# Kernel optimization log

Measured on AMD Instinct MI355X. Metric: run time of the kernel, lower is better.

Reference implementation:

```python
import jax, jax.numpy as jnp
import numpy as np

# Precompute flat gather indices replicating matA's banded structure.
# Row (layer l, offset i) of matA sums d[i : i+l], for l in 1..255, i in 0..255-l.
# Equivalently diff = cumsum_pad[i+l] - cumsum_pad[i].
def _build_indices():
    lo, hi, lid = [], [], []
    for l in range(1, 256):
        n = 256 - l
        i = np.arange(n)
        lo.append(i)
        hi.append(i + l)
        lid.append(np.full(n, l - 1))
    return (np.concatenate(lo), np.concatenate(hi), np.concatenate(lid))

_IDX_LO, _IDX_HI, _LAYER_ID = _build_indices()  # each length 32640
IDX_LO = jnp.asarray(_IDX_LO)
IDX_HI = jnp.asarray(_IDX_HI)
LAYER_ID = jnp.asarray(_LAYER_ID)
# elements averaged per layer: B * (256 - l)
_COUNTS = (256 - np.arange(1, 256)).astype(np.float32)
COUNTS = jnp.asarray(_COUNTS)


def setup_inputs() -> dict:
    key = jax.random.key(0)
    k1, k2, k3 = jax.random.split(key, 3)
    B = 512
    d1layer = jax.random.normal(k1, (B, 1, 255), dtype=jnp.float32)
    hvec = jax.random.normal(k2, (B, 32640), dtype=jnp.float32)
    mask = jax.random.uniform(k3, (B, 255), dtype=jnp.float32)
    return {"d1layer": d1layer, "hvec": hvec, "mask": mask}


def reference(d1layer, hvec, mask):
    B = d1layer.shape[0]
    m = jnp.power(mask, 2.5)  # [B, 255]
    d = d1layer[:, 0, :]  # [B, 255]
    # padded cumulative sum: c[:, k] = sum_{j<k} d[:, j], shape [B, 256]
    c = jnp.concatenate(
        [jnp.zeros((B, 1), dtype=d.dtype), jnp.cumsum(d, axis=1)], axis=1
    )
    # banded windowed sums for all 32640 (layer, offset) pairs at once
    matAd = c[:, IDX_HI] - c[:, IDX_LO]  # [B, 32640]
    w = m[:, LAYER_ID]  # [B, 32640], mask[:, layer-1] broadcast over offsets
    sq = jnp.square(matAd - hvec) * w  # [B, 32640]
    per_layer_sum = jax.ops.segment_sum(
        jnp.sum(sq, axis=0), LAYER_ID, num_segments=255
    )  # [255]
    loss_layers = per_layer_sum / (COUNTS * jnp.float32(B))  # per-layer mean
    return jnp.mean(loss_layers)
```

## Files before the change

### kernel.cpp

```cpp
#include <hip/hip_runtime.h>

#define NLAYER 255
#define SEQ    256
#define TOTJ   32640
#define CHUNKS 8
#define CHUNK_J (TOTJ / CHUNKS)
#define CHUNK_F4 (CHUNK_J / 4)
#define THREADS 256

__global__ void build_table(unsigned short* __restrict__ table) {
    int l = blockIdx.x + 1;
    int n = 256 - l;
    int i = threadIdx.x;
    if (i < n) {
        int base = 256 * (l - 1) - ((l - 1) * l) / 2;
        table[base + i] = (unsigned short)((l - 1) | (i << 8));
    }
}

__global__ __launch_bounds__(THREADS) void main_kernel(
        const float* __restrict__ d1layer,
        const float* __restrict__ hvec,
        const float* __restrict__ mask,
        const unsigned short* __restrict__ table,
        float* __restrict__ partials)
{
    __shared__ float c[SEQ];
    __shared__ float w[NLAYER];
    __shared__ float red[THREADS / 64];

    const int b     = blockIdx.y;
    const int chunk = blockIdx.x;
    const int t     = threadIdx.x;

    c[t] = (t > 0) ? d1layer[b * NLAYER + (t - 1)] : 0.0f;
    if (t < NLAYER) {
        float mk = mask[b * NLAYER + t];
        w[t] = mk * mk * sqrtf(mk) / (float)(NLAYER - t);
    }
    __syncthreads();

    #pragma unroll
    for (int off = 1; off < SEQ; off <<= 1) {
        float v   = c[t];
        float add = (t >= off) ? c[t - off] : 0.0f;
        __syncthreads();
        c[t] = v + add;
        __syncthreads();
    }

    const float4* hv4 =
        (const float4*)(hvec + (size_t)b * TOTJ + (size_t)chunk * CHUNK_J);
    const unsigned short* tb = table + chunk * CHUNK_J;

    float acc = 0.0f;
    for (int f4 = t; f4 < CHUNK_F4; f4 += THREADS) {
        float4 h = hv4[f4];
        ushort4 tv = *(const ushort4*)(tb + f4 * 4);

        int l0 = tv.x & 0xFF, lo0 = tv.x >> 8;
        int l1 = tv.y & 0xFF, lo1 = tv.y >> 8;
        int l2 = tv.z & 0xFF, lo2 = tv.z >> 8;
        int l3 = tv.w & 0xFF, lo3 = tv.w >> 8;

        float d0 = (c[lo0 + l0 + 1] - c[lo0]) - h.x;
        float d1 = (c[lo1 + l1 + 1] - c[lo1]) - h.y;
        float d2 = (c[lo2 + l2 + 1] - c[lo2]) - h.z;
        float d3 = (c[lo3 + l3 + 1] - c[lo3]) - h.w;

        acc += d0 * d0 * w[l0];
        acc += d1 * d1 * w[l1];
        acc += d2 * d2 * w[l2];
        acc += d3 * d3 * w[l3];
    }

    #pragma unroll
    for (int off = 32; off > 0; off >>= 1)
        acc += __shfl_down(acc, off, 64);
    int lane = t & 63, wid = t >> 6;
    if (lane == 0) red[wid] = acc;
    __syncthreads();
    if (t == 0) {
        float s = 0.0f;
        #pragma unroll
        for (int i = 0; i < THREADS / 64; ++i) s += red[i];
        partials[b * gridDim.x + chunk] = s;
    }
}

__global__ void reduce_kernel(const float* __restrict__ partials, int n, int B,
                              float* __restrict__ out) {
    __shared__ float red[16];
    float acc = 0.0f;
    for (int i = threadIdx.x; i < n; i += blockDim.x) acc += partials[i];
    #pragma unroll
    for (int off = 32; off > 0; off >>= 1)
        acc += __shfl_down(acc, off, 64);
    int lane = threadIdx.x & 63, wid = threadIdx.x >> 6;
    if (lane == 0) red[wid] = acc;
    __syncthreads();
    if (threadIdx.x == 0) {
        float s = 0.0f;
        int nw = blockDim.x >> 6;
        for (int i = 0; i < nw; ++i) s += red[i];
        out[0] = s / ((float)NLAYER * (float)B);
    }
}

extern "C" void kernel_launch(void* const* d_in, const int* in_sizes, int n_in,
                              void* d_out, int out_size, void* d_ws, size_t ws_size,
                              hipStream_t stream) {
    const float* d1layer = (const float*)d_in[0];
    const float* hvec    = (const float*)d_in[1];
    const float* mask    = (const float*)d_in[2];
    float* out = (float*)d_out;

    const int B = in_sizes[2] / NLAYER;

    unsigned short* table = (unsigned short*)d_ws;
    float* partials = (float*)((char*)d_ws + TOTJ * sizeof(unsigned short));

    build_table<<<NLAYER, 256, 0, stream>>>(table);

    dim3 grid(CHUNKS, B);
    main_kernel<<<grid, THREADS, 0, stream>>>(d1layer, hvec, mask, table, partials);

    reduce_kernel<<<1, 1024, 0, stream>>>(partials, CHUNKS * B, B, out);
}
```

Before: 104.7 us.

## Compute band indices analytically and fold final reduction into atomics

```diff
diff --git a/kernel.cpp b/kernel.cpp
--- a/kernel.cpp
+++ b/kernel.cpp
@@ -8,22 +8,12 @@
 #define CHUNK_F4 (CHUNK_J / 4)
 #define THREADS 256
 
-__global__ void build_table(unsigned short* __restrict__ table) {
-    int l = blockIdx.x + 1;
-    int n = 256 - l;
-    int i = threadIdx.x;
-    if (i < n) {
-        int base = 256 * (l - 1) - ((l - 1) * l) / 2;
-        table[base + i] = (unsigned short)((l - 1) | (i << 8));
-    }
-}
-
 __global__ __launch_bounds__(THREADS) void main_kernel(
         const float* __restrict__ d1layer,
         const float* __restrict__ hvec,
         const float* __restrict__ mask,
-        const unsigned short* __restrict__ table,
-        float* __restrict__ partials)
+        float* __restrict__ out,
+        float scale)
 {
     __shared__ float c[SEQ];
     __shared__ float w[NLAYER];
@@ -36,7 +26,7 @@
     c[t] = (t > 0) ? d1layer[b * NLAYER + (t - 1)] : 0.0f;
     if (t < NLAYER) {
         float mk = mask[b * NLAYER + t];
-        w[t] = mk * mk * sqrtf(mk) / (float)(NLAYER - t);
+        w[t] = mk * mk * sqrtf(mk) * scale / (float)(NLAYER - t);
     }
     __syncthreads();
 
@@ -51,27 +41,30 @@
 
     const float4* hv4 =
         (const float4*)(hvec + (size_t)b * TOTJ + (size_t)chunk * CHUNK_J);
-    const unsigned short* tb = table + chunk * CHUNK_J;
+    const int jbase = chunk * CHUNK_J;
 
     float acc = 0.0f;
     for (int f4 = t; f4 < CHUNK_F4; f4 += THREADS) {
         float4 h = hv4[f4];
-        ushort4 tv = *(const ushort4*)(tb + f4 * 4);
+        int j = jbase + f4 * 4;
 
-        int l0 = tv.x & 0xFF, lo0 = tv.x >> 8;
-        int l1 = tv.y & 0xFF, lo1 = tv.y >> 8;
-        int l2 = tv.z & 0xFF, lo2 = tv.z >> 8;
-        int l3 = tv.w & 0xFF, lo3 = tv.w >> 8;
+        float s = sqrtf((float)(261121 - 8 * j));
+        int k  = (int)((511.0f - s) * 0.5f);
+        int sk = (511 * k - k * k) >> 1;
+        int sk1 = sk + (NLAYER - k);
+        if (sk1 <= j) { k++; sk = sk1; }
+        if (sk > j)   { sk -= (NLAYER + 1 - k); k--; }
+        int lo = j - sk;
 
-        float d0 = (c[lo0 + l0 + 1] - c[lo0]) - h.x;
-        float d1 = (c[lo1 + l1 + 1] - c[lo1]) - h.y;
-        float d2 = (c[lo2 + l2 + 1] - c[lo2]) - h.z;
-        float d3 = (c[lo3 + l3 + 1] - c[lo3]) - h.w;
-
-        acc += d0 * d0 * w[l0];
-        acc += d1 * d1 * w[l1];
-        acc += d2 * d2 * w[l2];
-        acc += d3 * d3 * w[l3];
+        float hh[4] = {h.x, h.y, h.z, h.w};
+        #pragma unroll
+        for (int e = 0; e < 4; ++e) {
+            float dv = (c[lo + k + 1] - c[lo]) - hh[e];
+            acc = fmaf(dv * dv, w[k], acc);
+            int nxt = (lo + 1 == NLAYER - k) ? 1 : 0;
+            lo = nxt ? 0 : (lo + 1);
+            k += nxt;
+        }
     }
 
     #pragma unroll
@@ -81,29 +74,10 @@
     if (lane == 0) red[wid] = acc;
     __syncthreads();
     if (t == 0) {
-        float s = 0.0f;
+        float s2 = 0.0f;
         #pragma unroll
-        for (int i = 0; i < THREADS / 64; ++i) s += red[i];
-        partials[b * gridDim.x + chunk] = s;
-    }
-}
-
-__global__ void reduce_kernel(const float* __restrict__ partials, int n, int B,
-                              float* __restrict__ out) {
-    __shared__ float red[16];
-    float acc = 0.0f;
-    for (int i = threadIdx.x; i < n; i += blockDim.x) acc += partials[i];
-    #pragma unroll
-    for (int off = 32; off > 0; off >>= 1)
-        acc += __shfl_down(acc, off, 64);
-    int lane = threadIdx.x & 63, wid = threadIdx.x >> 6;
-    if (lane == 0) red[wid] = acc;
-    __syncthreads();
-    if (threadIdx.x == 0) {
-        float s = 0.0f;
-        int nw = blockDim.x >> 6;
-        for (int i = 0; i < nw; ++i) s += red[i];
-        out[0] = s / ((float)NLAYER * (float)B);
+        for (int i = 0; i < THREADS / 64; ++i) s2 += red[i];
+        atomicAdd(out, s2);
     }
 }
 
@@ -117,13 +91,9 @@
 
     const int B = in_sizes[2] / NLAYER;
 
-    unsigned short* table = (unsigned short*)d_ws;
-    float* partials = (float*)((char*)d_ws + TOTJ * sizeof(unsigned short));
+    hipMemsetAsync(out, 0, sizeof(float), stream);
 
-    build_table<<<NLAYER, 256, 0, stream>>>(table);
-
+    const float scale = 1.0f / ((float)NLAYER * (float)B);
     dim3 grid(CHUNKS, B);
-    main_kernel<<<grid, THREADS, 0, stream>>>(d1layer, hvec, mask, table, partials);
-
-    reduce_kernel<<<1, 1024, 0, stream>>>(partials, CHUNKS * B, B, out);
+    main_kernel<<<grid, THREADS, 0, stream>>>(d1layer, hvec, mask, out, scale);
 }
```

Result: slower. 141.6 us (+35.3%).
